# Kernel tuning notes

Hardware: AMD Instinct MI355X
Metric: run time of the kernel (lower is better)

Reference implementation:

```python
import jax, jax.numpy as jnp
import numpy as np

Y0 = 0.28209479177387814  # real spherical harmonic Y_0^0 = 1/(2*sqrt(pi))
KSIZE = 5
PAD = 2


def _radial_masks(kernel_size):
    """Binary masks, one per distinct squared radius in the kernel grid (matches
    _compute_spherical_coords_and_masks: voxels sharing r^2 share a mask)."""
    c = (kernel_size - 1) // 2
    g = np.arange(kernel_size) - c
    ii, jj, kk = np.meshgrid(g, g, g, indexing='ij')
    r2 = ii ** 2 + jj ** 2 + kk ** 2
    vals = np.unique(r2)
    return np.stack([(r2 == v).astype(np.float32) for v in vals], axis=0)  # [P,K,K,K]


def setup_inputs() -> dict:
    key = jax.random.key(0)
    k1, k2, k3 = jax.random.split(key, 3)
    masks = jnp.asarray(_radial_masks(KSIZE))              # [P=10, 5, 5, 5]
    P = masks.shape[0]
    x = jax.random.normal(k1, (2, 32, 1, 48, 48, 48), dtype=jnp.float32)
    weight = jax.random.normal(k2, (64, 32, 1, 1, 1, P), dtype=jnp.float32)
    bias = 0.1 * jax.random.normal(k3, (64,), dtype=jnp.float32)
    return {"x": x, "weight": weight, "bias": bias, "masks": masks}


def reference(x, weight, bias, masks):
    B, I = x.shape[0], x.shape[1]
    O = weight.shape[0]
    # Filter build (order_in=order_out=order_filter=1): CG_000 = 1, Y_0 constant.
    # F[o,i,x,y,z] = Y0 * sum_p W[o,i,p] * mask[p,x,y,z]
    filt = Y0 * jnp.einsum('oip,pxyz->oixyz', weight[:, :, 0, 0, 0, :], masks)
    xr = x.reshape(B, I * x.shape[2], *x.shape[3:])        # [B, I, D, H, W]
    out = jax.lax.conv_general_dilated(
        xr, filt, window_strides=(1, 1, 1), padding=[(PAD, PAD)] * 3,
        dimension_numbers=('NCDHW', 'OIDHW', 'NCDHW'))
    out = out.reshape(B, O, 1, *out.shape[2:])             # [B, O, 1, D, H, W]
    # bias added only to the l=0 irrep channel (index 0 of dim 2; size 1 here)
    return out + bias[None, :, None, None, None, None]
```

## Files before the change

### kernel.cpp

```cpp
#include <hip/hip_runtime.h>
#include <stdint.h>

#define V3 110592
#define PLANE 2304
#define NO 64

typedef unsigned short ushort_t;
typedef __attribute__((ext_vector_type(8))) short short8v;
typedef __attribute__((ext_vector_type(4))) float float4v;

__device__ __forceinline__ uint32_t f2bf1(float f) {
  uint32_t u = __float_as_uint(f);
  u += 0x7FFFu + ((u >> 16) & 1u);
  return u >> 16;
}
__device__ __forceinline__ uint32_t pack2(float a, float b) {
  return f2bf1(a) | (f2bf1(b) << 16);
}

__device__ __forceinline__ void prep_body(const float* __restrict__ w,
                                          ushort_t* __restrict__ Afr, int idx) {
  int r = idx & 7, m = (idx >> 3) & 63, g = idx >> 9;
  int kk = g * 8 + r;
  int dzi = kk / 192, k2 = kk % 192;
  int i = k2 / 6, qi = k2 % 6;
  const int Q[6] = {0, 1, 2, 4, 5, 8};
  const int pidx[13] = {0, 1, 2, 3, 4, 5, 6, 0, 7, 8, 0, 0, 9};
  int dz = dzi - 2;
  int p = pidx[Q[qi] + dz * dz];
  Afr[idx] = (ushort_t)f2bf1(0.28209479177387814f * w[(m * 32 + i) * 10 + p]);
}

__global__ __launch_bounds__(256, 4) void bq_kernel(const float* __restrict__ x,
                                                    ushort_t* __restrict__ Bq,
                                                    const float* __restrict__ w,
                                                    ushort_t* __restrict__ Afr,
                                                    int zbase) {
  const int tid = threadIdx.x;
  const int b = blockIdx.x;
  if (zbase == 0 && b < 240) prep_body(w, Afr, b * 256 + tid);

  const int q = b & 7;
  const int dg = q >> 1, half = q & 1;
  const int s = b >> 3;
  const int dl = s % 12;
  const int ig = (s / 12) & 7;
  const int z = zbase + s / 96;
  const int d = dg * 12 + dl;

  const int lane = tid & 63;
  const int strip = tid >> 6;
  const float* xb = x + (size_t)z * 32 * V3;
  ushort_t* Bqb = Bq + (size_t)z * ((size_t)1152 * PLANE * 8);

  const int h0 = (half * 4 + strip) * 6;
  const int gw = lane - 2;
  const bool okw = (gw >= 0 && gw < 48);
  const int sl1 = lane > 0 ? lane - 1 : 0;
  const int sl2 = lane > 1 ? lane - 2 : 0;
  const int sr1 = lane < 63 ? lane + 1 : 63;
  const int sr2 = lane < 62 ? lane + 2 : 63;
  const bool okst = (lane >= 2 && lane <= 49);

  const float* px[4];
#pragma unroll
  for (int ii = 0; ii < 4; ++ii)
    px[ii] = xb + ((size_t)(ig * 4 + ii) * 48 + d) * PLANE + gw;

  float v[10][4];
#pragma unroll
  for (int r = 0; r < 10; ++r) {
    const int gh = h0 - 2 + r;
    const bool okv = okw && (gh >= 0) && (gh < 48);
#pragma unroll
    for (int ii = 0; ii < 4; ++ii)
      v[r][ii] = okv ? px[ii][gh * 48] : 0.f;
  }

  float s1[4][5], s4[4][5];
#pragma unroll
  for (int r = 0; r < 10; ++r) {
    const int slot = r % 5;
#pragma unroll
    for (int ii = 0; ii < 4; ++ii) {
      float val = v[r][ii];
      float vl1 = __shfl(val, sl1);
      float vr1 = __shfl(val, sr1);
      float vl2 = __shfl(val, sl2);
      float vr2 = __shfl(val, sr2);
      s1[ii][slot] = vl1 + vr1;
      s4[ii][slot] = vl2 + vr2;
    }
    if (r >= 4) {
      const int j0 = (r - 4) % 5, j1 = (r - 3) % 5, j2 = (r - 2) % 5,
                j3 = (r - 1) % 5, j4 = r % 5;
      uint32_t dw[12];
#pragma unroll
      for (int ii = 0; ii < 4; ++ii) {
        float B0 = v[r - 2][ii];
        float B1 = s1[ii][j2] + v[r - 3][ii] + v[r - 1][ii];
        float B2 = s1[ii][j1] + s1[ii][j3];
        float B3 = s4[ii][j2] + v[r - 4][ii] + v[r][ii];
        float B4 = s4[ii][j1] + s4[ii][j3] + s1[ii][j0] + s1[ii][j4];
        float B5 = s4[ii][j0] + s4[ii][j4];
        dw[ii * 3 + 0] = pack2(B0, B1);
        dw[ii * 3 + 1] = pack2(B2, B3);
        dw[ii * 3 + 2] = pack2(B4, B5);
      }
      if (okst) {
        const int n = (h0 + r - 4) * 48 + gw;
        const size_t gb = (size_t)(d * 24 + ig * 3);
        uint4 c0 = {dw[0], dw[1], dw[2], dw[3]};
        uint4 c1 = {dw[4], dw[5], dw[6], dw[7]};
        uint4 c2 = {dw[8], dw[9], dw[10], dw[11]};
        *(uint4*)(Bqb + ((gb + 0) * PLANE + n) * 8) = c0;
        *(uint4*)(Bqb + ((gb + 1) * PLANE + n) * 8) = c1;
        *(uint4*)(Bqb + ((gb + 2) * PLANE + n) * 8) = c2;
      }
    }
  }
}

__global__ __launch_bounds__(256, 4) void gemm_kernel(const ushort_t* __restrict__ Bq,
                                                      const ushort_t* __restrict__ Afr,
                                                      const float* __restrict__ bias,
                                                      float* __restrict__ out) {
  const int tid = threadIdx.x;
  const int lane = tid & 63, wi = tid >> 6;
  const int quad = lane >> 4, m15 = lane & 15;
  const int b = blockIdx.x;
  const int p = b & 7;
  const int s = b >> 3;
  const int dl = s / 9;
  const int nbl = s - dl * 9;
  const int d = (p >> 1) * 12 + dl;
  const int n0 = ((p & 1) * 9 + nbl) * 128 + wi * 32;
  const ushort_t* Bqb = Bq + (size_t)blockIdx.z * ((size_t)1152 * PLANE * 8);
  float* outb = out + (size_t)blockIdx.z * (size_t)NO * V3;

  const int lo = (d < 2) ? (2 - d) : 0;
  const int hi = (d > 45) ? (49 - d) : 4;
  const int kslo = 6 * lo;
  const int T = 6 * (hi - lo + 1);

  const ushort_t* ap = Afr + ((size_t)(kslo * 4 + quad) * 64 + m15) * 8;
  const ushort_t* bp = Bqb + ((size_t)((d - 2) * 24 + kslo * 4 + quad) * PLANE + n0 + m15) * 8;
  const int astep = 4 * 64 * 8;
  const int bstep = 4 * PLANE * 8;

  float4v acc[4][2];
#pragma unroll
  for (int mt = 0; mt < 4; ++mt)
#pragma unroll
    for (int nt = 0; nt < 2; ++nt) acc[mt][nt] = (float4v){0.f, 0.f, 0.f, 0.f};

  short8v A0[4], B0[2], A1[4], B1[2], A2[4], B2[2];

#define SBAR __builtin_amdgcn_sched_barrier(0)
#define LOADSET(Ax, Bx)                                                        \
  {                                                                            \
    _Pragma("unroll") for (int nt = 0; nt < 2; ++nt)                           \
        Bx[nt] = *(const short8v*)(bp + nt * 128);                             \
    _Pragma("unroll") for (int mt = 0; mt < 4; ++mt)                           \
        Ax[mt] = *(const short8v*)(ap + mt * 128);                             \
    ap += astep; bp += bstep;                                                  \
  }
#define MFMASET(Ax, Bx)                                                        \
  {                                                                            \
    __builtin_amdgcn_s_setprio(1);                                             \
    _Pragma("unroll") for (int mt = 0; mt < 4; ++mt)                           \
        _Pragma("unroll") for (int nt = 0; nt < 2; ++nt)                       \
            acc[mt][nt] = __builtin_amdgcn_mfma_f32_16x16x32_bf16(             \
                Ax[mt], Bx[nt], acc[mt][nt], 0, 0, 0);                         \
    __builtin_amdgcn_s_setprio(0);                                             \
  }

  LOADSET(A0, B0);
  LOADSET(A1, B1);
  SBAR;
  for (int k = 0; k < T - 3; k += 3) {
    LOADSET(A2, B2); SBAR;
    MFMASET(A0, B0); SBAR;
    LOADSET(A0, B0); SBAR;
    MFMASET(A1, B1); SBAR;
    LOADSET(A1, B1); SBAR;
    MFMASET(A2, B2); SBAR;
  }
  LOADSET(A2, B2); SBAR;
  MFMASET(A0, B0);
  MFMASET(A1, B1);
  MFMASET(A2, B2);
#undef LOADSET
#undef MFMASET
#undef SBAR

  const int vb = d * PLANE + n0 + m15;
#pragma unroll
  for (int mt = 0; mt < 4; ++mt) {
#pragma unroll
    for (int r = 0; r < 4; ++r) {
      int m = mt * 16 + quad * 4 + r;
      float bv = bias[m];
      float* op = outb + (size_t)m * V3 + vb;
#pragma unroll
      for (int nt = 0; nt < 2; ++nt)
        __builtin_nontemporal_store(acc[mt][nt][r] + bv, op + nt * 16);
    }
  }
}

extern "C" void kernel_launch(void* const* d_in, const int* in_sizes, int n_in,
                              void* d_out, int out_size, void* d_ws, size_t ws_size,
                              hipStream_t stream) {
  const float* x    = (const float*)d_in[0];
  const float* w    = (const float*)d_in[1];
  const float* bias = (const float*)d_in[2];
  float* out = (float*)d_out;

  ushort_t* Afr = (ushort_t*)d_ws;
  ushort_t* Bq  = (ushort_t*)((char*)d_ws + 131072);
  const size_t SB = (size_t)1152 * PLANE * 8 * 2;
  const bool both = (ws_size >= 131072 + 2 * SB);

  if (both) {
    bq_kernel<<<dim3(1536), 256, 0, stream>>>(x, Bq, w, Afr, 0);
    gemm_kernel<<<dim3(864, 1, 2), 256, 0, stream>>>(Bq, Afr, bias, out);
  } else {
    for (int b = 0; b < 2; ++b) {
      bq_kernel<<<dim3(768), 256, 0, stream>>>(x + (size_t)b * 32 * V3, Bq, w, Afr, 0);
      gemm_kernel<<<dim3(864, 1, 1), 256, 0, stream>>>(Bq, Afr, bias,
                                                       out + (size_t)b * NO * V3);
    }
  }
}
```

Baseline: 149.0 us.

## Stage GEMM weight fragments into LDS with double-buffered async loads

The GEMM kernel now stages the weight (A) fragments for each dz slice into shared memory with global_load_lds, double-buffered across dz iterations, and reads them from LDS rather than having every wave load them from global memory. The B operand moves to a simple one-step register prefetch, replacing the three-set software pipeline and its sched barriers. The goal is to cut redundant global/L2 traffic for A, since all four waves share the same weights. In exchange it adds 48KB of LDS per block, a __syncthreads per slice and lowers launch bounds to 3 blocks per CU, which may reduce occupancy and latency hiding for the B loads.

```diff
diff --git a/kernel.cpp b/kernel.cpp
--- a/kernel.cpp
+++ b/kernel.cpp
@@ -121,7 +121,7 @@
   }
 }
 
-__global__ __launch_bounds__(256, 4) void gemm_kernel(const ushort_t* __restrict__ Bq,
+__global__ __launch_bounds__(256, 3) void gemm_kernel(const ushort_t* __restrict__ Bq,
                                                       const ushort_t* __restrict__ Afr,
                                                       const float* __restrict__ bias,
                                                       float* __restrict__ out) {
@@ -140,12 +140,21 @@
 
   const int lo = (d < 2) ? (2 - d) : 0;
   const int hi = (d > 45) ? (49 - d) : 4;
-  const int kslo = 6 * lo;
-  const int T = 6 * (hi - lo + 1);
-
-  const ushort_t* ap = Afr + ((size_t)(kslo * 4 + quad) * 64 + m15) * 8;
-  const ushort_t* bp = Bqb + ((size_t)((d - 2) * 24 + kslo * 4 + quad) * PLANE + n0 + m15) * 8;
-  const int astep = 4 * 64 * 8;
+
+  __shared__ ushort_t sA[2][12288];
+
+#define STAGE(DZI, BUF)                                                        \
+  {                                                                            \
+    const ushort_t* src_ = Afr + (size_t)(DZI) * 12288 + tid * 8;              \
+    ushort_t* dst_ = &sA[BUF][(tid >> 6) * 512];                               \
+    _Pragma("unroll") for (int r_ = 0; r_ < 6; ++r_)                           \
+        __builtin_amdgcn_global_load_lds(                                      \
+            (const __attribute__((address_space(1))) void*)(src_ + r_ * 2048), \
+            (__attribute__((address_space(3))) void*)(dst_ + r_ * 2048),       \
+            16, 0, 0);                                                         \
+  }
+
+  const ushort_t* bp = Bqb + ((size_t)((d - 2) * 24 + 6 * lo * 4 + quad) * PLANE + n0 + m15) * 8;
   const int bstep = 4 * PLANE * 8;
 
   float4v acc[4][2];
@@ -154,45 +163,45 @@
 #pragma unroll
     for (int nt = 0; nt < 2; ++nt) acc[mt][nt] = (float4v){0.f, 0.f, 0.f, 0.f};
 
-  short8v A0[4], B0[2], A1[4], B1[2], A2[4], B2[2];
-
-#define SBAR __builtin_amdgcn_sched_barrier(0)
-#define LOADSET(Ax, Bx)                                                        \
-  {                                                                            \
-    _Pragma("unroll") for (int nt = 0; nt < 2; ++nt)                           \
-        Bx[nt] = *(const short8v*)(bp + nt * 128);                             \
-    _Pragma("unroll") for (int mt = 0; mt < 4; ++mt)                           \
-        Ax[mt] = *(const short8v*)(ap + mt * 128);                             \
-    ap += astep; bp += bstep;                                                  \
-  }
-#define MFMASET(Ax, Bx)                                                        \
-  {                                                                            \
-    __builtin_amdgcn_s_setprio(1);                                             \
-    _Pragma("unroll") for (int mt = 0; mt < 4; ++mt)                           \
-        _Pragma("unroll") for (int nt = 0; nt < 2; ++nt)                       \
-            acc[mt][nt] = __builtin_amdgcn_mfma_f32_16x16x32_bf16(             \
-                Ax[mt], Bx[nt], acc[mt][nt], 0, 0, 0);                         \
-    __builtin_amdgcn_s_setprio(0);                                             \
-  }
-
-  LOADSET(A0, B0);
-  LOADSET(A1, B1);
-  SBAR;
-  for (int k = 0; k < T - 3; k += 3) {
-    LOADSET(A2, B2); SBAR;
-    MFMASET(A0, B0); SBAR;
-    LOADSET(A0, B0); SBAR;
-    MFMASET(A1, B1); SBAR;
-    LOADSET(A1, B1); SBAR;
-    MFMASET(A2, B2); SBAR;
-  }
-  LOADSET(A2, B2); SBAR;
-  MFMASET(A0, B0);
-  MFMASET(A1, B1);
-  MFMASET(A2, B2);
-#undef LOADSET
-#undef MFMASET
-#undef SBAR
+  short8v Bc[2], Bn[2];
+
+  STAGE(lo, 0);
+#pragma unroll
+  for (int nt = 0; nt < 2; ++nt) Bc[nt] = *(const short8v*)(bp + nt * 128);
+  bp += bstep;
+  __syncthreads();
+
+  int buf = 0;
+  for (int dzi = lo; dzi <= hi; ++dzi) {
+    if (dzi < hi) STAGE(dzi + 1, buf ^ 1);
+    const ushort_t* sAb = &sA[buf][(size_t)quad * 512 + m15 * 8];
+#pragma unroll
+    for (int ks = 0; ks < 6; ++ks) {
+      const bool last = (dzi == hi) && (ks == 5);
+      if (!last) {
+#pragma unroll
+        for (int nt = 0; nt < 2; ++nt) Bn[nt] = *(const short8v*)(bp + nt * 128);
+        bp += bstep;
+      }
+      short8v a0 = *(const short8v*)(sAb + ks * 2048 + 0 * 128);
+      short8v a1 = *(const short8v*)(sAb + ks * 2048 + 1 * 128);
+      short8v a2 = *(const short8v*)(sAb + ks * 2048 + 2 * 128);
+      short8v a3 = *(const short8v*)(sAb + ks * 2048 + 3 * 128);
+      __builtin_amdgcn_s_setprio(1);
+#pragma unroll
+      for (int nt = 0; nt < 2; ++nt) {
+        acc[0][nt] = __builtin_amdgcn_mfma_f32_16x16x32_bf16(a0, Bc[nt], acc[0][nt], 0, 0, 0);
+        acc[1][nt] = __builtin_amdgcn_mfma_f32_16x16x32_bf16(a1, Bc[nt], acc[1][nt], 0, 0, 0);
+        acc[2][nt] = __builtin_amdgcn_mfma_f32_16x16x32_bf16(a2, Bc[nt], acc[2][nt], 0, 0, 0);
+        acc[3][nt] = __builtin_amdgcn_mfma_f32_16x16x32_bf16(a3, Bc[nt], acc[3][nt], 0, 0, 0);
+      }
+      __builtin_amdgcn_s_setprio(0);
+      Bc[0] = Bn[0]; Bc[1] = Bn[1];
+    }
+    __syncthreads();
+    buf ^= 1;
+  }
+#undef STAGE
 
   const int vb = d * PLANE + n0 + m15;
 #pragma unroll
```

After: 145.0 us, median of 2. 1.03x faster.
